# Optimization experiments

Hardware: AMD Instinct MI355X
Metric: run time of the kernel (lower is better)

The kernel has to match this reference:

```python
import jax, jax.numpy as jnp
import numpy as np

B, L, D = 2, 2048, 2048
H = 16
DH = D // H  # 128
EPS = 1e-6


def _rope_cos_sin(seq_len, dim, dtype):
    inv_freq = 1.0 / (10000.0 ** (jnp.arange(0, dim, 2, dtype=jnp.float32) / dim))
    t = jnp.arange(seq_len, dtype=jnp.float32)
    freqs = jnp.einsum('i,j->ij', t, inv_freq)          # [L, dim/2]
    emb = jnp.concatenate([freqs, freqs], axis=-1)      # [L, dim]
    return jnp.cos(emb).astype(dtype)[None, None], jnp.sin(emb).astype(dtype)[None, None]


def _rotate_half(x):
    x1, x2 = jnp.split(x, 2, axis=-1)
    return jnp.concatenate([-x2, x1], axis=-1)


def _rms_norm(x, w):
    var = jnp.mean(jnp.square(x), axis=-1, keepdims=True)
    return x * jax.lax.rsqrt(var + EPS) * w


def setup_inputs() -> dict:
    key = jax.random.key(0)
    ks = jax.random.split(key, 4)
    s_in = 1.0 / np.sqrt(D)
    return {
        'x': jax.random.normal(ks[0], (B, L, D), jnp.float32),
        'attention_mask': jnp.zeros((B, 1, 1, L), jnp.bool_),
        'Wqkv': jax.random.normal(ks[1], (D, 3 * D), jnp.float32) * s_in,
        'bqkv': jnp.zeros((3 * D,), jnp.float32),
        'Wout': jax.random.normal(ks[2], (D, D), jnp.float32) * s_in,
        'bout': jnp.zeros((D,), jnp.float32),
        'q_norm_w': jnp.ones((DH,), jnp.float32),
        'k_norm_w': jnp.ones((DH,), jnp.float32),
    }


def reference(x, attention_mask, Wqkv, bqkv, Wout, bout, q_norm_w, k_norm_w):
    b, l, d = x.shape
    qkv = x @ Wqkv + bqkv                                   # [B,L,3D]
    q, k, v = jnp.split(qkv, 3, axis=-1)
    # [B,H,L,DH]
    q = q.reshape(b, l, H, DH).transpose(0, 2, 1, 3)
    k = k.reshape(b, l, H, DH).transpose(0, 2, 1, 3)
    v = v.reshape(b, l, H, DH).transpose(0, 2, 1, 3)

    cos, sin = _rope_cos_sin(l, DH, x.dtype)
    q = q * cos + _rotate_half(q) * sin
    k = k * cos + _rotate_half(k) * sin

    q = _rms_norm(q, q_norm_w)
    k = _rms_norm(k, k_norm_w)

    # SDPA with additive (float-cast) mask, as in the original code
    scale = 1.0 / np.sqrt(DH)
    scores = jnp.einsum('bhqd,bhkd->bhqk', q, k) * scale
    scores = scores + attention_mask.astype(x.dtype)        # broadcast [B,1,1,L]
    attn = jax.nn.softmax(scores, axis=-1)
    out = jnp.einsum('bhqk,bhkd->bhqd', attn, v)            # [B,H,L,DH]

    # zero out masked query rows: padding_mask = mask.transpose(2,3) -> [B,1,L,1]
    padding_mask = jnp.swapaxes(attention_mask, 2, 3)
    out = jnp.where(padding_mask, 0.0, out)

    out = out.transpose(0, 2, 1, 3).reshape(b, l, d)
    return out @ Wout + bout
```

## Files before the change

kernel.cpp:

```cpp
#include <hip/hip_runtime.h>
#include <hip/hip_bf16.h>

typedef __bf16 bf16;
using bf16x8 = __attribute__((ext_vector_type(8))) __bf16;
using bf16x4 = __attribute__((ext_vector_type(4))) __bf16;
using f32x4  = __attribute__((ext_vector_type(4))) float;
using f32x16 = __attribute__((ext_vector_type(16))) float;

#define DEV __device__ __forceinline__

DEV void load_lds16(const void* g, void* l) {
  __builtin_amdgcn_global_load_lds(
      (const __attribute__((address_space(1))) void*)g,
      (__attribute__((address_space(3))) void*)l, 16, 0, 0);
}

__global__ __launch_bounds__(256) void k_prep(
    const float* __restrict__ x, bf16* __restrict__ xb,
    const float* __restrict__ Wq, bf16* __restrict__ wqT,
    const float* __restrict__ Wo, bf16* __restrict__ woT,
    float* __restrict__ invf) {
  __shared__ float t[64][65];
  int bid = blockIdx.x;
  int tid = threadIdx.x;
  if (bid < 4096) {
    long i = ((long)bid * 256 + tid) * 8;
    float4 a = *(const float4*)(x + i);
    float4 b = *(const float4*)(x + i + 4);
    bf16x8 o;
    o[0] = (bf16)a.x; o[1] = (bf16)a.y; o[2] = (bf16)a.z; o[3] = (bf16)a.w;
    o[4] = (bf16)b.x; o[5] = (bf16)b.y; o[6] = (bf16)b.z; o[7] = (bf16)b.w;
    *(bf16x8*)(xb + i) = o;
    return;
  }
  if (bid >= 8192) {
    if (tid < 64) invf[tid] = 1.0f / (float)pow(10000.0, (double)tid / 64.0);
    return;
  }
  const float* in;
  bf16* out;
  int R, C, rb;
  if (bid < 7168) { in = Wq; out = wqT; R = 2048; C = 6144; rb = bid - 4096; }
  else            { in = Wo; out = woT; R = 2048; C = 2048; rb = bid - 7168; }
  int nbc = C >> 6;
  long r0 = (long)(rb / nbc) * 64, c0 = (long)(rb % nbc) * 64;
#pragma unroll
  for (int i = 0; i < 4; ++i) {
    int ch = tid + i * 256;
    int r = ch >> 4, c4 = (ch & 15) * 4;
    float4 v = *(const float4*)(in + (r0 + r) * C + c0 + c4);
    t[r][c4] = v.x; t[r][c4 + 1] = v.y; t[r][c4 + 2] = v.z; t[r][c4 + 3] = v.w;
  }
  __syncthreads();
#pragma unroll
  for (int i = 0; i < 2; ++i) {
    int ch = tid + i * 256;
    int c = ch >> 3, r8 = (ch & 7) * 8;
    bf16x8 o;
#pragma unroll
    for (int j = 0; j < 8; ++j) o[j] = (bf16)t[r8 + j][c];
    *(bf16x8*)(out + (c0 + c) * R + r0 + r8) = o;
  }
}

__global__ __launch_bounds__(512, 1) void k_gemm8q(
    const bf16* __restrict__ A, const bf16* __restrict__ Bt,
    const float* __restrict__ bias,
    const float* __restrict__ invf,
    const float* __restrict__ qw, const float* __restrict__ kw,
    bf16* __restrict__ q_r, bf16* __restrict__ k_r, bf16* __restrict__ v_t) {
  __shared__ __align__(16) bf16 ls[2][2][256 * 64];
  int bid = blockIdx.x;
  { int q = gridDim.x >> 3; bid = (bid & 7) * q + (bid >> 3); }
  const int bm = bid & 15, bn = bid >> 4;
  const int tid = threadIdx.x, lane = tid & 63, w = tid >> 6;
  const int wm = w >> 2, wn = w & 3;
  const int fr = lane & 15, fq = lane >> 4;
  const long abase = (long)bm * 256 * 2048;
  const long bbase = (long)bn * 256 * 2048;
  f32x4 acc[8][4] = {};
  bf16x8 bfv[4][2];

#define STG(op, GP, gb, kt, hf)                                                \
  { _Pragma("unroll") for (int it2 = 0; it2 < 2; ++it2) {                      \
      int g = it2 * 512 + tid;                                                 \
      int rl = g >> 3, u = g & 7;                                              \
      load_lds16(GP + gb + (long)((hf) * 128 + rl) * 2048 + ((kt) << 6)        \
                     + ((u ^ (rl & 7)) << 3),                                  \
                 &ls[op][(kt) & 1][(hf) * 8192 + g * 8]);                      \
  } }

#define PH(qd, slot, STGCODE)                                                  \
  {                                                                            \
    bf16x8 afv[2][2];                                                          \
    _Pragma("unroll") for (int mm = 0; mm < 2; ++mm)                           \
      _Pragma("unroll") for (int kk = 0; kk < 2; ++kk) {                       \
        int R = wm * 128 + ((qd) * 2 + mm) * 16 + fr;                          \
        afv[mm][kk] = *(const bf16x8*)&ls[0][slot]                             \
            [R * 64 + (((kk * 4 + fq) ^ (R & 7)) << 3)];                       \
      }                                                                        \
    if ((qd) == 0) {                                                           \
      _Pragma("unroll") for (int nn = 0; nn < 4; ++nn)                         \
        _Pragma("unroll") for (int kk = 0; kk < 2; ++kk) {                     \
          int R = wn * 64 + nn * 16 + fr;                                      \
          bfv[nn][kk] = *(const bf16x8*)&ls[1][slot]                           \
              [R * 64 + (((kk * 4 + fq) ^ (R & 7)) << 3)];                     \
        }                                                                      \
    }                                                                          \
    STGCODE                                                                    \
    __builtin_amdgcn_s_barrier();                                              \
    asm volatile("s_waitcnt lgkmcnt(0)" ::: "memory");                         \
    __builtin_amdgcn_s_setprio(1);                                             \
    _Pragma("unroll") for (int mm = 0; mm < 2; ++mm)                           \
      _Pragma("unroll") for (int nn = 0; nn < 4; ++nn)                         \
        _Pragma("unroll") for (int kk = 0; kk < 2; ++kk)                       \
          acc[(qd) * 2 + mm][nn] = __builtin_amdgcn_mfma_f32_16x16x32_bf16(    \
              afv[mm][kk], bfv[nn][kk], acc[(qd) * 2 + mm][nn], 0, 0, 0);      \
    __builtin_amdgcn_s_setprio(0);                                             \
    __builtin_amdgcn_s_barrier();                                              \
  }

  STG(1, Bt, bbase, 0, 0) STG(1, Bt, bbase, 0, 1)
  STG(0, A, abase, 0, 0)  STG(0, A, abase, 0, 1)
  STG(1, Bt, bbase, 1, 0) STG(1, Bt, bbase, 1, 1)

  for (int u = 0; u < 16; ++u) {
    const int t = 2 * u;
    asm volatile("s_waitcnt vmcnt(4)" ::: "memory");
    __builtin_amdgcn_s_barrier();
    PH(0, 0, STG(0, A, abase, t + 1, 0))
    PH(1, 0, STG(0, A, abase, t + 1, 1))
    PH(2, 0, if (u < 15) { STG(1, Bt, bbase, t + 2, 0) })
    PH(3, 0, if (u < 15) { STG(1, Bt, bbase, t + 2, 1) })
    if (u < 15) { asm volatile("s_waitcnt vmcnt(4)" ::: "memory"); }
    else        { asm volatile("s_waitcnt vmcnt(0)" ::: "memory"); }
    __builtin_amdgcn_s_barrier();
    PH(0, 1, if (u < 15) { STG(0, A, abase, t + 2, 0) })
    PH(1, 1, if (u < 15) { STG(0, A, abase, t + 2, 1) })
    PH(2, 1, if (u < 15) { STG(1, Bt, bbase, t + 3, 0) })
    PH(3, 1, if (u < 15) { STG(1, Bt, bbase, t + 3, 1) })
  }
#undef PH
#undef STG

  bf16* tile = &ls[0][0][0];
  const int b = bm >> 3, l0 = (bm & 7) << 8;

  if (bn < 16) {
#pragma unroll
    for (int n = 0; n < 4; ++n) {
      int col = wn * 64 + n * 16 + fr;
      float bv = bias[bn * 256 + col];
#pragma unroll
      for (int m = 0; m < 8; ++m)
#pragma unroll
        for (int r = 0; r < 4; ++r) {
          int row = wm * 128 + m * 16 + fq * 4 + r;
          tile[row * 256 + (col ^ ((row & 7) << 3))] = (bf16)(acc[m][n][r] + bv);
        }
    }
    __syncthreads();
    const float* wv = (bn < 8) ? qw : kw;
    bf16* dst0 = (bn < 8) ? q_r : k_r;
    const int tc = tid & 15, hh = (tid >> 4) & 1, rgrp = tid >> 5, i8 = tc * 8;
    const int hg = (bn & 7) * 2 + hh;
    const bool lo = i8 < 64;
    float wvv[8], invv[8];
#pragma unroll
    for (int j = 0; j < 8; ++j) wvv[j] = wv[i8 + j];
#pragma unroll
    for (int j = 0; j < 8; ++j) invv[j] = invf[(i8 + j) & 63];
#pragma unroll
    for (int it = 0; it < 16; ++it) {
      int row = it * 16 + rgrp;
      float fl = (float)(l0 + row);
      float cc[8], sn[8];
#pragma unroll
      for (int j = 0; j < 8; ++j) __sincosf(fl * invv[j], &sn[j], &cc[j]);
      int colb = hh * 128 + i8;
      bf16x8 xv = *(const bf16x8*)&tile[row * 256 + (colb ^ ((row & 7) << 3))];
      float v[8], p[8], rr[8];
      float ss = 0.f;
#pragma unroll
      for (int j = 0; j < 8; ++j) v[j] = (float)xv[j];
#pragma unroll
      for (int j = 0; j < 8; ++j) p[j] = __shfl_xor(v[j], 8);
#pragma unroll
      for (int j = 0; j < 8; ++j) {
        rr[j] = lo ? v[j] * cc[j] - p[j] * sn[j] : v[j] * cc[j] + p[j] * sn[j];
        ss += rr[j] * rr[j];
      }
      ss += __shfl_xor(ss, 1);
      ss += __shfl_xor(ss, 2);
      ss += __shfl_xor(ss, 4);
      ss += __shfl_xor(ss, 8);
      float inv = rsqrtf(ss * (1.f / 128.f) + 1e-6f);
      bf16x8 ov;
#pragma unroll
      for (int j = 0; j < 8; ++j) ov[j] = (bf16)(rr[j] * inv * wvv[j]);
      *(bf16x8*)(dst0 + ((long)((b * 16 + hg) * 2048 + (l0 + row))) * 128 + i8) = ov;
    }
  } else {
#pragma unroll
    for (int n = 0; n < 4; ++n) {
      int col = wn * 64 + n * 16 + fr;
      float bv = bias[bn * 256 + col];
#pragma unroll
      for (int m = 0; m < 8; ++m)
#pragma unroll
        for (int r = 0; r < 4; ++r) {
          int row = wm * 128 + m * 16 + fq * 4 + r;
          tile[col * 256 + (row ^ ((col & 7) << 3))] = (bf16)(acc[m][n][r] + bv);
        }
    }
    __syncthreads();
#pragma unroll
    for (int it = 0; it < 16; ++it) {
      int ch = it * 512 + tid;
      int d = ch >> 5, l8 = (ch & 31) * 8;
      int hg = (bn - 16) * 2 + (d >> 7), dl = d & 127;
      bf16x8 vv = *(const bf16x8*)&tile[d * 256 + (l8 ^ ((d & 7) << 3))];
      *(bf16x8*)(v_t + ((long)((b * 16 + hg) * 128 + dl)) * 2048 + l0 + l8) = vv;
    }
  }
}

__global__ __launch_bounds__(512, 1) void k_g8out(
    const bf16* __restrict__ A, const bf16* __restrict__ Bt,
    const float* __restrict__ bias, float* __restrict__ C,
    int M, int N, int K) {
  __shared__ __align__(16) bf16 ls[3 * 8192 + 3 * 16384];
  bf16* lsA = ls;
  bf16* lsB = ls + 3 * 8192;
  int bid = blockIdx.x;
  { int q = gridDim.x >> 3; bid = (bid & 7) * q + (bid >> 3); }
  const int nbm = M >> 7;
  const int bm = bid % nbm, bn = bid / nbm;
  const int tid = threadIdx.x, lane = tid & 63, w = tid >> 6;
  const int wm = w >> 2, wn = w & 3;
  const int fr = lane & 15, fq = lane >> 4;
  const long abase = (long)bm * 128 * K;
  const long bbase = (long)bn * 256 * K;
  const int NT = K >> 6;
  f32x4 acc[4][4] = {};
  bf16x8 bfv[4][2];

#define STGA(sl, kt)                                                           \
  { _Pragma("unroll") for (int i2 = 0; i2 < 2; ++i2) {                         \
      int g = i2 * 512 + tid;                                                  \
      int rl = g >> 3, uu = g & 7;                                             \
      load_lds16(A + abase + (long)rl * K + ((kt) << 6) + ((uu ^ (rl & 7)) << 3), \
                 &lsA[(sl) * 8192 + g * 8]); } }
#define STGB(sl, kt, i0, i1)                                                   \
  { _Pragma("unroll") for (int i2 = i0; i2 < i1; ++i2) {                       \
      int g = i2 * 512 + tid;                                                  \
      int rl = g >> 3, uu = g & 7;                                             \
      load_lds16(Bt + bbase + (long)rl * K + ((kt) << 6) + ((uu ^ (rl & 7)) << 3), \
                 &lsB[(sl) * 16384 + g * 8]); } }

  STGA(0, 0) STGB(0, 0, 0, 4)
  STGA(1, 1) STGB(1, 1, 0, 4)

  for (int t = 0; t < NT; ++t) {
    const int sl = t % 3, s2 = (t + 2) % 3;
    if (t < NT - 1) asm volatile("s_waitcnt vmcnt(6)" ::: "memory");
    else            asm volatile("s_waitcnt vmcnt(0)" ::: "memory");
    __builtin_amdgcn_s_barrier();
    {
      bf16x8 af0[2][2];
#pragma unroll
      for (int mm = 0; mm < 2; ++mm)
#pragma unroll
        for (int kk = 0; kk < 2; ++kk) {
          int R = wm * 64 + mm * 16 + fr;
          af0[mm][kk] = *(const bf16x8*)&lsA[sl * 8192 + R * 64 + (((kk * 4 + fq) ^ (R & 7)) << 3)];
        }
#pragma unroll
      for (int nn = 0; nn < 4; ++nn)
#pragma unroll
        for (int kk = 0; kk < 2; ++kk) {
          int R = wn * 64 + nn * 16 + fr;
          bfv[nn][kk] = *(const bf16x8*)&lsB[sl * 16384 + R * 64 + (((kk * 4 + fq) ^ (R & 7)) << 3)];
        }
      if (t + 2 < NT) { STGA(s2, t + 2) STGB(s2, t + 2, 0, 2) }
      __builtin_amdgcn_s_barrier();
      asm volatile("s_waitcnt lgkmcnt(0)" ::: "memory");
      __builtin_amdgcn_s_setprio(1);
#pragma unroll
      for (int mm = 0; mm < 2; ++mm)
#pragma unroll
        for (int nn = 0; nn < 4; ++nn)
#pragma unroll
          for (int kk = 0; kk < 2; ++kk)
            acc[mm][nn] = __builtin_amdgcn_mfma_f32_16x16x32_bf16(af0[mm][kk], bfv[nn][kk],
                                                                  acc[mm][nn], 0, 0, 0);
      __builtin_amdgcn_s_setprio(0);
      __builtin_amdgcn_s_barrier();
    }
    {
      bf16x8 af1[2][2];
#pragma unroll
      for (int mm = 0; mm < 2; ++mm)
#pragma unroll
        for (int kk = 0; kk < 2; ++kk) {
          int R = wm * 64 + (2 + mm) * 16 + fr;
          af1[mm][kk] = *(const bf16x8*)&lsA[sl * 8192 + R * 64 + (((kk * 4 + fq) ^ (R & 7)) << 3)];
        }
      if (t + 2 < NT) { STGB(s2, t + 2, 2, 4) }
      __builtin_amdgcn_s_barrier();
      asm volatile("s_waitcnt lgkmcnt(0)" ::: "memory");
      __builtin_amdgcn_s_setprio(1);
#pragma unroll
      for (int mm = 0; mm < 2; ++mm)
#pragma unroll
        for (int nn = 0; nn < 4; ++nn)
#pragma unroll
          for (int kk = 0; kk < 2; ++kk)
            acc[2 + mm][nn] = __builtin_amdgcn_mfma_f32_16x16x32_bf16(af1[mm][kk], bfv[nn][kk],
                                                                      acc[2 + mm][nn], 0, 0, 0);
      __builtin_amdgcn_s_setprio(0);
      __builtin_amdgcn_s_barrier();
    }
  }
#undef STGA
#undef STGB

#pragma unroll
  for (int nn = 0; nn < 4; ++nn) {
    int col = bn * 256 + wn * 64 + nn * 16 + fr;
    float bv = bias[col];
#pragma unroll
    for (int m = 0; m < 4; ++m) {
      int row0 = bm * 128 + wm * 64 + m * 16 + fq * 4;
#pragma unroll
      for (int r = 0; r < 4; ++r)
        C[(long)(row0 + r) * N + col] = acc[m][nn][r] + bv;
    }
  }
}

__global__ __launch_bounds__(512, 1) void k_attn(
    const bf16* __restrict__ q_r, const bf16* __restrict__ k_r,
    const bf16* __restrict__ v_t, const unsigned char* __restrict__ amask,
    bf16* __restrict__ attno) {
  __shared__ __align__(16) bf16 lK[2][64 * 128];
  __shared__ __align__(16) bf16 lV[3][128 * 64];
  __shared__ int sAny;
  const int tid = threadIdx.x, lane = tid & 63, w = tid >> 6;
  const int hi = lane >> 5, q31 = lane & 31;
  const int bh = blockIdx.x & 31, qt = blockIdx.x >> 5;
  const int b = bh >> 4, h = bh & 15;
  const long hbase = (long)bh * 2048 * 128;
  const int q0 = qt * 256 + w * 32;
  const unsigned char* mb = amask + b * 2048;

  if (tid == 0) sAny = 0;
  __syncthreads();
  {
    unsigned mv = *(const unsigned*)(mb + tid * 4);
    if (mv) sAny = 1;
  }

  bf16x8 qf[8];
#pragma unroll
  for (int ksl = 0; ksl < 8; ++ksl)
    qf[ksl] = *(const bf16x8*)(q_r + hbase + (long)(q0 + q31) * 128 + ksl * 16 + hi * 8);

  f32x16 o[4] = {};
  float m_run = -1e30f, l_run = 0.f;
  const float SC2 = 0.08838834764831845f * 1.4426950408889634f;
  const float L2E = 1.4426950408889634f;

#define STAGE_K(buf, kv0)                                                            \
  {                                                                                  \
    _Pragma("unroll") for (int it = 0; it < 2; ++it) {                               \
      int g = it * 512 + w * 64 + lane;                                              \
      int r = g >> 4, u = g & 15;                                                    \
      load_lds16(k_r + hbase + (long)((kv0) + r) * 128 + ((u ^ (r & 7)) << 3),       \
                 &lK[buf][(it * 512 + w * 64) * 8]);                                 \
    }                                                                                \
  }
#define STAGE_V(buf, kv0)                                                            \
  {                                                                                  \
    _Pragma("unroll") for (int it = 0; it < 2; ++it) {                               \
      int g = it * 512 + w * 64 + lane;                                              \
      int r = g >> 3, u = g & 7;                                                     \
      load_lds16(v_t + hbase + (long)r * 2048 + (kv0) + ((u ^ (r & 7)) << 3),        \
                 &lV[buf][(it * 512 + w * 64) * 8]);                                 \
    }                                                                                \
  }

  STAGE_K(0, 0) STAGE_V(0, 0) STAGE_K(1, 64) STAGE_V(1, 64)
  __syncthreads();
  const bool maskAny = sAny != 0;

  f32x16 st0 = {}, st1 = {};
#pragma unroll
  for (int ksl = 0; ksl < 8; ++ksl) {
    const int u = ksl * 2 + hi;
    bf16x8 kf0 = *(const bf16x8*)&lK[0][q31 * 128 + ((u ^ (q31 & 7)) << 3)];
    bf16x8 kf1 = *(const bf16x8*)&lK[0][(32 + q31) * 128 + ((u ^ (q31 & 7)) << 3)];
    st0 = __builtin_amdgcn_mfma_f32_32x32x16_bf16(kf0, qf[ksl], st0, 0, 0, 0);
    st1 = __builtin_amdgcn_mfma_f32_32x32x16_bf16(kf1, qf[ksl], st1, 0, 0, 0);
  }
  __syncthreads();

  for (int t = 0; t < 32; ++t) {
    const int kv0 = t << 6;
    if (t + 2 < 32) {
      STAGE_K(t & 1, kv0 + 128)
      STAGE_V((t + 2) % 3, kv0 + 128)
    }

    f32x16 sn0 = {}, sn1 = {};
    if (t < 31) {
      const bf16* kb = lK[(t + 1) & 1];
#pragma unroll
      for (int ksl = 0; ksl < 8; ++ksl) {
        const int u = ksl * 2 + hi;
        bf16x8 kf0 = *(const bf16x8*)&kb[q31 * 128 + ((u ^ (q31 & 7)) << 3)];
        bf16x8 kf1 = *(const bf16x8*)&kb[(32 + q31) * 128 + ((u ^ (q31 & 7)) << 3)];
        sn0 = __builtin_amdgcn_mfma_f32_32x32x16_bf16(kf0, qf[ksl], sn0, 0, 0, 0);
        sn1 = __builtin_amdgcn_mfma_f32_32x32x16_bf16(kf1, qf[ksl], sn1, 0, 0, 0);
      }
    }

#pragma unroll
    for (int i = 0; i < 16; ++i) { st0[i] *= SC2; st1[i] *= SC2; }
    if (maskAny) {
#pragma unroll
      for (int i = 0; i < 16; ++i) {
        int c = (i & 3) + 8 * (i >> 2) + 4 * hi;
        if (mb[kv0 + c]) st0[i] += L2E;
        if (mb[kv0 + 32 + c]) st1[i] += L2E;
      }
    }
    float tm = st0[0];
#pragma unroll
    for (int i = 1; i < 16; ++i) tm = fmaxf(tm, st0[i]);
#pragma unroll
    for (int i = 0; i < 16; ++i) tm = fmaxf(tm, st1[i]);
    tm = fmaxf(tm, __shfl_xor(tm, 32));

    if (!__all(tm <= m_run + 8.f)) {
      float mn = fmaxf(m_run, tm);
      float corr = exp2f(m_run - mn);
      m_run = mn;
      l_run *= corr;
#pragma unroll
      for (int i = 0; i < 16; ++i) {
        float cr = __shfl(corr, (i & 3) + 8 * (i >> 2) + 4 * hi);
#pragma unroll
        for (int dt = 0; dt < 4; ++dt) o[dt][i] *= cr;
      }
    }

    float rs = 0.f;
#pragma unroll
    for (int i = 0; i < 16; ++i) { st0[i] = exp2f(st0[i] - m_run); rs += st0[i]; }
#pragma unroll
    for (int i = 0; i < 16; ++i) { st1[i] = exp2f(st1[i] - m_run); rs += st1[i]; }
    rs += __shfl_xor(rs, 32);
    l_run += rs;

    union UU { bf16x4 v; uint2 u; };
    union U8 { bf16x8 v; uint4 u; };
    bf16x8 pa[4];
#define MKPA(pidx, STX, bb)                                                          \
  {                                                                                  \
    UU plo, phi;                                                                     \
    plo.v = (bf16x4){(bf16)STX[bb], (bf16)STX[(bb) + 1], (bf16)STX[(bb) + 2],        \
                     (bf16)STX[(bb) + 3]};                                           \
    phi.v = (bf16x4){(bf16)STX[(bb) + 4], (bf16)STX[(bb) + 5], (bf16)STX[(bb) + 6],  \
                     (bf16)STX[(bb) + 7]};                                           \
    unsigned sx = hi ? plo.u.x : phi.u.x, sy = hi ? plo.u.y : phi.u.y;               \
    unsigned rx = (unsigned)__shfl_xor((int)sx, 32), ry = (unsigned)__shfl_xor((int)sy, 32); \
    U8 f;                                                                            \
    f.u.x = hi ? rx : plo.u.x; f.u.y = hi ? ry : plo.u.y;                            \
    f.u.z = hi ? phi.u.x : rx; f.u.w = hi ? phi.u.y : ry;                            \
    pa[pidx] = f.v;                                                                  \
  }
    MKPA(0, st0, 0) MKPA(1, st0, 8) MKPA(2, st1, 0) MKPA(3, st1, 8)
#undef MKPA

    const bf16* vb3 = lV[t % 3];
#pragma unroll
    for (int dt = 0; dt < 4; ++dt) {
      const int dr = dt * 32 + q31;
#pragma unroll
      for (int ks = 0; ks < 4; ++ks) {
        const int u = ks * 2 + hi;
        bf16x8 vb = *(const bf16x8*)&vb3[dr * 64 + ((u ^ (dr & 7)) << 3)];
        o[dt] = __builtin_amdgcn_mfma_f32_32x32x16_bf16(pa[ks], vb, o[dt], 0, 0, 0);
      }
    }

    __syncthreads();
    st0 = sn0;
    st1 = sn1;
  }
#undef STAGE_K
#undef STAGE_V

  float invl = 1.f / l_run;
#pragma unroll
  for (int i = 0; i < 16; ++i) {
    int q = (i & 3) + 8 * (i >> 2) + 4 * hi;
    int qrow = q0 + q;
    float inv = __shfl(invl, q);
    float zm = inv;
    if (maskAny) { if (mb[qrow]) zm = 0.f; }
#pragma unroll
    for (int dt = 0; dt < 4; ++dt)
      attno[(long)(b * 2048 + qrow) * 2048 + h * 128 + dt * 32 + q31] = (bf16)(o[dt][i] * zm);
  }
}

extern "C" void kernel_launch(void* const* d_in, const int* in_sizes, int n_in,
                              void* d_out, int out_size, void* d_ws, size_t ws_size,
                              hipStream_t stream) {
  const float* x = (const float*)d_in[0];
  const unsigned char* amask = (const unsigned char*)d_in[1];
  const float* Wqkv = (const float*)d_in[2];
  const float* bqkv = (const float*)d_in[3];
  const float* Wout = (const float*)d_in[4];
  const float* bout = (const float*)d_in[5];
  const float* qw = (const float*)d_in[6];
  const float* kw = (const float*)d_in[7];
  float* out = (float*)d_out;
  char* ws = (char*)d_ws;

  bf16* xb   = (bf16*)(ws);
  bf16* wqT  = (bf16*)(ws + 16777216);
  bf16* woT  = (bf16*)(ws + 41943040);
  bf16* q_r  = (bf16*)(ws + 100663296);
  bf16* k_r  = (bf16*)(ws + 117440512);
  bf16* v_t  = (bf16*)(ws + 134217728);
  float* invf = (float*)(ws + 150994944);
  bf16* attno = xb;

  k_prep<<<8193, 256, 0, stream>>>(x, xb, Wqkv, wqT, Wout, woT, invf);
  k_gemm8q<<<384, 512, 0, stream>>>(xb, wqT, bqkv, invf, qw, kw, q_r, k_r, v_t);
  k_attn<<<256, 512, 0, stream>>>(q_r, k_r, v_t, amask, attno);
  k_g8out<<<256, 512, 0, stream>>>(attno, woT, bout, out, 4096, 2048, 2048);
}
```

Measured before the change: 289.4 us.

## Triple-buffer A tiles in QKV GEMM to prefetch two k-steps ahead

Changes the QKV projection GEMM's LDS staging from double buffering of A and B to a triple-buffered A (modulo 3) plus double-buffered B. The loop now issues A loads two k-tiles ahead and waits on vmcnt(8) instead of vmcnt(4), which gives global-to-LDS loads more time to land behind the MFMA work. LDS use grows from 128KB to 160KB per block, and the loop is no longer manually unrolled by two, so slot indices are computed at runtime.

```diff
diff --git a/kernel.cpp b/kernel.cpp
--- a/kernel.cpp
+++ b/kernel.cpp
@@ -69,7 +69,9 @@
     const float* __restrict__ invf,
     const float* __restrict__ qw, const float* __restrict__ kw,
     bf16* __restrict__ q_r, bf16* __restrict__ k_r, bf16* __restrict__ v_t) {
-  __shared__ __align__(16) bf16 ls[2][2][256 * 64];
+  __shared__ __align__(16) bf16 ls[5 * 16384];
+  bf16* lsA = ls;
+  bf16* lsB = ls + 3 * 16384;
   int bid = blockIdx.x;
   { int q = gridDim.x >> 3; bid = (bid & 7) * q + (bid >> 3); }
   const int bm = bid & 15, bn = bid >> 4;
@@ -81,30 +83,38 @@
   f32x4 acc[8][4] = {};
   bf16x8 bfv[4][2];
 
-#define STG(op, GP, gb, kt, hf)                                                \
+#define STGA(kt, hf)                                                           \
   { _Pragma("unroll") for (int it2 = 0; it2 < 2; ++it2) {                      \
       int g = it2 * 512 + tid;                                                 \
       int rl = g >> 3, u = g & 7;                                              \
-      load_lds16(GP + gb + (long)((hf) * 128 + rl) * 2048 + ((kt) << 6)        \
+      load_lds16(A + abase + (long)((hf) * 128 + rl) * 2048 + ((kt) << 6)      \
                      + ((u ^ (rl & 7)) << 3),                                  \
-                 &ls[op][(kt) & 1][(hf) * 8192 + g * 8]);                      \
+                 &lsA[((kt) % 3) * 16384 + (hf) * 8192 + g * 8]);              \
   } }
-
-#define PH(qd, slot, STGCODE)                                                  \
+#define STGB(kt, hf)                                                           \
+  { _Pragma("unroll") for (int it2 = 0; it2 < 2; ++it2) {                      \
+      int g = it2 * 512 + tid;                                                 \
+      int rl = g >> 3, u = g & 7;                                              \
+      load_lds16(Bt + bbase + (long)((hf) * 128 + rl) * 2048 + ((kt) << 6)     \
+                     + ((u ^ (rl & 7)) << 3),                                  \
+                 &lsB[((kt) & 1) * 16384 + (hf) * 8192 + g * 8]);              \
+  } }
+
+#define PH(qd, sa, sb, STGCODE)                                                \
   {                                                                            \
     bf16x8 afv[2][2];                                                          \
     _Pragma("unroll") for (int mm = 0; mm < 2; ++mm)                           \
       _Pragma("unroll") for (int kk = 0; kk < 2; ++kk) {                       \
         int R = wm * 128 + ((qd) * 2 + mm) * 16 + fr;                          \
-        afv[mm][kk] = *(const bf16x8*)&ls[0][slot]                             \
-            [R * 64 + (((kk * 4 + fq) ^ (R & 7)) << 3)];                       \
+        afv[mm][kk] = *(const bf16x8*)&lsA[(sa) * 16384                        \
+            + R * 64 + (((kk * 4 + fq) ^ (R & 7)) << 3)];                      \
       }                                                                        \
     if ((qd) == 0) {                                                           \
       _Pragma("unroll") for (int nn = 0; nn < 4; ++nn)                         \
         _Pragma("unroll") for (int kk = 0; kk < 2; ++kk) {                     \
           int R = wn * 64 + nn * 16 + fr;                                      \
-          bfv[nn][kk] = *(const bf16x8*)&ls[1][slot]                           \
-              [R * 64 + (((kk * 4 + fq) ^ (R & 7)) << 3)];                     \
+          bfv[nn][kk] = *(const bf16x8*)&lsB[(sb) * 16384                      \
+              + R * 64 + (((kk * 4 + fq) ^ (R & 7)) << 3)];                    \
         }                                                                      \
     }                                                                          \
     STGCODE                                                                    \
@@ -120,30 +130,24 @@
     __builtin_amdgcn_s_barrier();                                              \
   }
 
-  STG(1, Bt, bbase, 0, 0) STG(1, Bt, bbase, 0, 1)
-  STG(0, A, abase, 0, 0)  STG(0, A, abase, 0, 1)
-  STG(1, Bt, bbase, 1, 0) STG(1, Bt, bbase, 1, 1)
-
-  for (int u = 0; u < 16; ++u) {
-    const int t = 2 * u;
-    asm volatile("s_waitcnt vmcnt(4)" ::: "memory");
+  STGA(0, 0) STGA(0, 1) STGB(0, 0) STGB(0, 1)
+  STGA(1, 0) STGA(1, 1) STGB(1, 0) STGB(1, 1)
+
+  for (int t = 0; t < 32; ++t) {
+    const int sa = t % 3, sb = t & 1;
+    if (t < 31) asm volatile("s_waitcnt vmcnt(8)" ::: "memory");
+    else        asm volatile("s_waitcnt vmcnt(0)" ::: "memory");
     __builtin_amdgcn_s_barrier();
-    PH(0, 0, STG(0, A, abase, t + 1, 0))
-    PH(1, 0, STG(0, A, abase, t + 1, 1))
-    PH(2, 0, if (u < 15) { STG(1, Bt, bbase, t + 2, 0) })
-    PH(3, 0, if (u < 15) { STG(1, Bt, bbase, t + 2, 1) })
-    if (u < 15) { asm volatile("s_waitcnt vmcnt(4)" ::: "memory"); }
-    else        { asm volatile("s_waitcnt vmcnt(0)" ::: "memory"); }
-    __builtin_amdgcn_s_barrier();
-    PH(0, 1, if (u < 15) { STG(0, A, abase, t + 2, 0) })
-    PH(1, 1, if (u < 15) { STG(0, A, abase, t + 2, 1) })
-    PH(2, 1, if (u < 15) { STG(1, Bt, bbase, t + 3, 0) })
-    PH(3, 1, if (u < 15) { STG(1, Bt, bbase, t + 3, 1) })
+    PH(0, sa, sb, if (t < 30) { STGA(t + 2, 0) })
+    PH(1, sa, sb, if (t < 30) { STGA(t + 2, 1) })
+    PH(2, sa, sb, if (t < 30) { STGB(t + 2, 0) })
+    PH(3, sa, sb, if (t < 30) { STGB(t + 2, 1) })
   }
 #undef PH
-#undef STG
-
-  bf16* tile = &ls[0][0][0];
+#undef STGA
+#undef STGB
+
+  bf16* tile = ls;
   const int b = bm >> 3, l0 = (bm & 7) << 8;
 
   if (bn < 16) {
```

After: 293.5 us. About the same (+1.4%).
